# Kernel tuning notes

Measured on AMD Instinct MI355X. Metric: run time of the kernel, lower is better.

Reference implementation:

```python
import jax, jax.numpy as jnp
import numpy as np

D_MODEL, D_STATE, D_CONV, D_INNER, DT_RANK, K = 96, 16, 3, 192, 6, 4
B, H, W = 1, 64, 64


def setup_inputs() -> dict:
    key = jax.random.key(0)
    ks = jax.random.split(key, 10)
    x = jax.random.normal(ks[0], (B, H, W, D_MODEL), jnp.float32)
    in_proj_w = jax.random.normal(ks[1], (2 * D_INNER, D_MODEL), jnp.float32) * 0.02
    conv_w = jax.random.normal(ks[2], (D_INNER, 1, D_CONV, D_CONV), jnp.float32) * 0.1
    conv_b = jnp.zeros((D_INNER,), jnp.float32)
    x_proj_w = jax.random.normal(ks[3], (K, DT_RANK + 2 * D_STATE, D_INNER), jnp.float32) * 0.02
    dt_std = DT_RANK ** -0.5
    dt_w = jax.random.uniform(ks[4], (K, D_INNER, DT_RANK), jnp.float32, -dt_std, dt_std)
    # dt bias init: inv-softplus of dt ~ logUniform(1e-3, 1e-1)
    u = jax.random.uniform(ks[5], (K, D_INNER), jnp.float32)
    dt = jnp.exp(u * (np.log(0.1) - np.log(0.001)) + np.log(0.001)).clip(1e-4)
    dt_b = dt + jnp.log(-jnp.expm1(-dt))
    A_logs = jnp.log(jnp.broadcast_to(jnp.arange(1, D_STATE + 1, dtype=jnp.float32), (K * D_INNER, D_STATE)))
    Ds = jnp.ones((K * D_INNER,), jnp.float32)
    ln_g = jnp.ones((D_INNER,), jnp.float32)
    ln_b = jnp.zeros((D_INNER,), jnp.float32)
    out_proj_w = jax.random.normal(ks[6], (D_MODEL, D_INNER), jnp.float32) * 0.02
    return dict(x=x, in_proj_w=in_proj_w, conv_w=conv_w, conv_b=conv_b, x_proj_w=x_proj_w,
                dt_w=dt_w, dt_b=dt_b, A_logs=A_logs, Ds=Ds, ln_g=ln_g, ln_b=ln_b,
                out_proj_w=out_proj_w)


def _ss2d(x, in_proj_w, conv_w, conv_b, x_proj_w, dt_w, dt_b, A_logs, Ds, ln_g, ln_b, out_proj_w):
    b, h, w, c = x.shape
    L = h * w
    d = conv_w.shape[0]            # d_inner
    n = A_logs.shape[1]            # d_state
    r = dt_w.shape[2]              # dt_rank
    # in_proj + split
    xz = jnp.einsum('bhwc,ec->bhwe', x, in_proj_w)
    xx, z = xz[..., :d], xz[..., d:]
    # depthwise conv (NCHW) + SiLU
    xc = xx.transpose(0, 3, 1, 2)
    pad = (D_CONV - 1) // 2
    xc = jax.lax.conv_general_dilated(xc, conv_w, (1, 1), [(pad, pad), (pad, pad)],
                                      feature_group_count=d) + conv_b[None, :, None, None]
    xc = jax.nn.silu(xc)
    # 4 scan directions: HW, WH, and their reverses
    x_hw = xc.reshape(b, d, L)
    x_wh = xc.transpose(0, 1, 3, 2).reshape(b, d, L)
    xs = jnp.stack([x_hw, x_wh, x_hw[..., ::-1], x_wh[..., ::-1]], axis=1)  # (b,K,d,L)
    x_dbl = jnp.einsum('bkdl,kcd->bkcl', xs, x_proj_w)
    dts, Bs, Cs = x_dbl[:, :, :r], x_dbl[:, :, r:r + n], x_dbl[:, :, r + n:]
    dts = jnp.einsum('bkrl,kdr->bkdl', dts, dt_w)
    delta = jax.nn.softplus(dts + dt_b[None, :, :, None])        # (b,K,d,L)
    A = -jnp.exp(A_logs).reshape(K, d, n)
    # time-major scanned inputs
    dA = jnp.exp(jnp.einsum('bkdl,kdn->lbkdn', delta, A))        # (L,b,K,d,n)
    dBu = jnp.einsum('bkdl,bknl,bkdl->lbkdn', delta, Bs, xs)
    Ct = Cs.transpose(3, 0, 1, 2)                                # (L,b,K,n)
    def step(hst, inp):
        dA_t, dBu_t, C_t = inp
        hst = dA_t * hst + dBu_t
        return hst, jnp.einsum('bkdn,bkn->bkd', hst, C_t)
    h0 = jnp.zeros((b, K, d, n), jnp.float32)
    _, ys = jax.lax.scan(step, h0, (dA, dBu, Ct))                # ys: (L,b,K,d)
    out_y = ys.transpose(1, 2, 3, 0) + xs * Ds.reshape(K, d)[None, :, :, None]
    # recombine directions
    inv = out_y[:, 2:4][..., ::-1]
    y1 = out_y[:, 0]
    y2 = inv[:, 0]
    wh = out_y[:, 1].reshape(b, d, w, h).transpose(0, 1, 3, 2).reshape(b, d, L)
    invwh = inv[:, 1].reshape(b, d, w, h).transpose(0, 1, 3, 2).reshape(b, d, L)
    y = (y1 + y2 + wh + invwh).transpose(0, 2, 1).reshape(b, h, w, d)
    # LayerNorm (eps=1e-5, torch default)
    mu = y.mean(-1, keepdims=True)
    var = ((y - mu) ** 2).mean(-1, keepdims=True)
    y = (y - mu) * jax.lax.rsqrt(var + 1e-5) * ln_g + ln_b
    y = y * jax.nn.silu(z)
    return jnp.einsum('bhwd,cd->bhwc', y, out_proj_w)


def reference(x, in_proj_w, conv_w, conv_b, x_proj_w, dt_w, dt_b, A_logs, Ds, ln_g, ln_b, out_proj_w):
    return _ss2d(x, in_proj_w, conv_w, conv_b, x_proj_w, dt_w, dt_b, A_logs, Ds, ln_g, ln_b, out_proj_w)
```

## Files before the change

### kernel.cpp

```cpp
#include <hip/hip_runtime.h>
#include <hip/hip_bf16.h>

#define LL 4096
#define DM 96
#define DI 192
#define NS 16
#define RK 6
#define RKP 8
#define KD 4
#define CPROJ 38
#define NC (KD*DI*NS)
#define PT 32
#define WS 196
#define OT 16
#define L2E 1.44269504f

__device__ __forceinline__ float b2f(__hip_bfloat16 v){ return __bfloat162float(v); }

__device__ __forceinline__ int detect_bf16(const unsigned short* __restrict__ xh, int tid, int* sflag){
  if (tid < 64){
    unsigned short u = xh[2*tid];
    int e = (u >> 7) & 0xFF;
    int sane = (e >= 107 && e <= 131) ? 1 : 0;
    unsigned long long m = __ballot(sane);
    if (tid == 0) *sflag = (__popcll(m) >= 32) ? 1 : 0;
  }
  return 0;
}

struct P12 { const void* p[12]; };
__global__ void k_convert_all(P12 ptrs, float* __restrict__ dst) {
  const int off[13] = {0,393216,430080,431808,432000,461184,465792,466560,
                       478848,479616,479808,480000,498432};
  __shared__ int sflag;
  detect_bf16((const unsigned short*)ptrs.p[0], threadIdx.x, &sflag);
  __syncthreads();
  int f = sflag;
  int i = blockIdx.x * 256 + threadIdx.x;
  if (i >= 498432) return;
  int j = 0;
  #pragma unroll
  for (int s = 1; s < 12; s++) if (i >= off[s]) j = s;
  int e = i - off[j];
  if (f) dst[i] = b2f(((const __hip_bfloat16*)ptrs.p[j])[e]);
  else   dst[i] = ((const float*)ptrs.p[j])[e];
}

__global__ void k_inproj(const float* __restrict__ x,
                         const float* __restrict__ w,
                         float* __restrict__ xx, float* __restrict__ z) {
  __shared__ float xr[8*DM];
  int l0 = blockIdx.x * 8;
  int tid = threadIdx.x;
  for (int i = tid; i < 8*DM; i += 384) xr[i] = x[l0*DM + i];
  __syncthreads();
  int e = tid;
  float acc[8];
  #pragma unroll
  for (int i=0;i<8;i++) acc[i]=0.f;
  const float* wr = w + e*DM;
  for (int c=0;c<DM;c++){
    float wv = wr[c];
    #pragma unroll
    for (int i=0;i<8;i++) acc[i] = fmaf(wv, xr[i*DM+c], acc[i]);
  }
  if (e < DI) {
    #pragma unroll
    for (int i=0;i<8;i++) xx[(l0+i)*DI + e] = acc[i];
  } else {
    int e2 = e - DI;
    #pragma unroll
    for (int i=0;i<8;i++) z[(l0+i)*DI + e2] = acc[i];
  }
}

__global__ void k_conv(const float* __restrict__ xx,
                       const float* __restrict__ cw,
                       const float* __restrict__ cb,
                       float* __restrict__ xc) {
  int l = blockIdx.x;
  int d = threadIdx.x;
  int h = l >> 6, w = l & 63;
  float acc = cb[d];
  #pragma unroll
  for (int ki=0; ki<3; ki++){
    int hh = h + ki - 1;
    if ((unsigned)hh >= 64u) continue;
    #pragma unroll
    for (int kj=0;kj<3;kj++){
      int wj = w + kj - 1;
      if ((unsigned)wj >= 64u) continue;
      acc = fmaf(cw[d*9 + ki*3 + kj], xx[(hh*64+wj)*DI + d], acc);
    }
  }
  xc[l*DI + d] = acc / (1.f + __expf(-acc));
}

__device__ __forceinline__ int dir_map(int k, int t){
  if (k==0) return t;
  if (k==1) return ((t&63)<<6) | (t>>6);
  if (k==2) return 4095 - t;
  int u = 4095 - t; return ((u&63)<<6) | (u>>6);
}

__global__ void __launch_bounds__(256) k_proj(const float* __restrict__ xc,
                       const float* __restrict__ xpw,
                       float* __restrict__ dts,
                       float* __restrict__ Bb, float* __restrict__ Cb,
                       float* __restrict__ yacc) {
  __shared__ float wl[CPROJ*WS];
  __shared__ float xs[PT*WS];
  int b = blockIdx.x;
  int k = b >> 7;
  int t_base = (b & 127) * PT;
  int tid = threadIdx.x;
  if (k == 0){
    float4* yz = (float4*)(yacc + (size_t)t_base*DI);
    for (int idx = tid; idx < PT*DI/4; idx += 256)
      yz[idx] = make_float4(0.f,0.f,0.f,0.f);
  }
  for (int idx = tid; idx < CPROJ*DI; idx += 256){
    int cc = idx / DI, j = idx - cc*DI;
    wl[cc*WS + j] = xpw[(k*CPROJ + cc)*DI + j];
  }
  for (int idx = tid; idx < PT*DI; idx += 256){
    int tt = idx / DI, j = idx - tt*DI;
    xs[tt*WS + j] = xc[dir_map(k, t_base + tt)*DI + j];
  }
  __syncthreads();
  int tg = tid & 7;
  int ty = tid >> 3;
  int cc0 = ty;
  int has2 = (ty + 32 < CPROJ);
  int cc1 = has2 ? (ty + 32) : ty;
  float a0x=0.f,a0y=0.f,a0z=0.f,a0w=0.f;
  float a1x=0.f,a1y=0.f,a1z=0.f,a1w=0.f;
  const float4* w0p = (const float4*)&wl[cc0*WS];
  const float4* w1p = (const float4*)&wl[cc1*WS];
  const float4* x0p = (const float4*)&xs[(tg     )*WS];
  const float4* x1p = (const float4*)&xs[(tg +  8)*WS];
  const float4* x2p = (const float4*)&xs[(tg + 16)*WS];
  const float4* x3p = (const float4*)&xs[(tg + 24)*WS];
  #pragma unroll 4
  for (int jc = 0; jc < DI/4; jc++){
    float4 w0 = w0p[jc], w1 = w1p[jc];
    float4 x0 = x0p[jc], x1 = x1p[jc], x2 = x2p[jc], x3 = x3p[jc];
    a0x = fmaf(w0.x,x0.x,fmaf(w0.y,x0.y,fmaf(w0.z,x0.z,fmaf(w0.w,x0.w,a0x))));
    a0y = fmaf(w0.x,x1.x,fmaf(w0.y,x1.y,fmaf(w0.z,x1.z,fmaf(w0.w,x1.w,a0y))));
    a0z = fmaf(w0.x,x2.x,fmaf(w0.y,x2.y,fmaf(w0.z,x2.z,fmaf(w0.w,x2.w,a0z))));
    a0w = fmaf(w0.x,x3.x,fmaf(w0.y,x3.y,fmaf(w0.z,x3.z,fmaf(w0.w,x3.w,a0w))));
    a1x = fmaf(w1.x,x0.x,fmaf(w1.y,x0.y,fmaf(w1.z,x0.z,fmaf(w1.w,x0.w,a1x))));
    a1y = fmaf(w1.x,x1.x,fmaf(w1.y,x1.y,fmaf(w1.z,x1.z,fmaf(w1.w,x1.w,a1y))));
    a1z = fmaf(w1.x,x2.x,fmaf(w1.y,x2.y,fmaf(w1.z,x2.z,fmaf(w1.w,x2.w,a1z))));
    a1w = fmaf(w1.x,x3.x,fmaf(w1.y,x3.y,fmaf(w1.z,x3.z,fmaf(w1.w,x3.w,a1w))));
  }
  float accs0[4] = {a0x,a0y,a0z,a0w};
  float accs1[4] = {a1x,a1y,a1z,a1w};
  #pragma unroll
  for (int i=0;i<4;i++){
    int t = t_base + tg + 8*i;
    size_t kt = (size_t)k*LL + t;
    {
      int cc = cc0; float v = accs0[i];
      if (cc < RK)            dts[kt*RKP + cc] = v;
      else if (cc < RK+NS)    Bb [kt*NS + (cc-RK)] = v;
      else                    Cb [kt*NS + (cc-RK-NS)] = v;
    }
    if (has2){
      int cc = ty + 32; float v = accs1[i];
      if (cc < RK+NS)         Bb [kt*NS + (cc-RK)] = v;
      else                    Cb [kt*NS + (cc-RK-NS)] = v;
    }
  }
}

template<int CHB>
__global__ void __launch_bounds__(256) k_scan1(
                      const float* __restrict__ xc,
                      const float* __restrict__ dts,
                      const float* __restrict__ Bbuf,
                      const float* __restrict__ A_logs,
                      const float* __restrict__ dtw,
                      const float* __restrict__ dtb,
                      float* __restrict__ Pb, float* __restrict__ Hb) {
  constexpr int CS = LL >> CHB;
  int b = blockIdx.x;
  int c = b & ((1<<CHB)-1);
  int kg = b >> CHB;
  int k = kg / 3, dg3 = kg - k*3;
  int tid = threadIdx.x;
  int dl = tid >> 2, nq = tid & 3;
  int d = dg3*64 + dl;
  int kd = k*DI + d;
  float4 Al = *(const float4*)&A_logs[kd*NS + nq*4];
  float A0 = -__expf(Al.x)*L2E, A1 = -__expf(Al.y)*L2E;
  float A2 = -__expf(Al.z)*L2E, A3 = -__expf(Al.w)*L2E;
  float bt = dtb[kd];
  float w0 = dtw[kd*RK+0], w1 = dtw[kd*RK+1], w2 = dtw[kd*RK+2];
  float w3 = dtw[kd*RK+3], w4 = dtw[kd*RK+4], w5 = dtw[kd*RK+5];
  const float* dr = dts + ((size_t)k*LL + c*CS)*RKP;
  const float4* bp = (const float4*)(Bbuf + ((size_t)k*LL + c*CS)*NS) + nq;
  float h0=0.f,h1=0.f,h2=0.f,h3=0.f, P0=1.f,P1=1.f,P2=1.f,P3=1.f;
  for (int s=0; s<CS; s++){
    int t = c*CS + s;
    float4 lo = *(const float4*)(dr + s*RKP);
    float4 hi = *(const float4*)(dr + s*RKP + 4);
    float v = bt;
    v = fmaf(w0, lo.x, v); v = fmaf(w1, lo.y, v); v = fmaf(w2, lo.z, v);
    v = fmaf(w3, lo.w, v); v = fmaf(w4, hi.x, v); v = fmaf(w5, hi.y, v);
    float sp = (v > 20.f) ? v : __logf(1.f + __expf(v));
    float sx = sp * xc[dir_map(k,t)*DI + d];
    float4 bv = bp[s*4];
    float a;
    a = exp2f(sp*A0); h0 = fmaf(a, h0, sx*bv.x); P0 *= a;
    a = exp2f(sp*A1); h1 = fmaf(a, h1, sx*bv.y); P1 *= a;
    a = exp2f(sp*A2); h2 = fmaf(a, h2, sx*bv.z); P2 *= a;
    a = exp2f(sp*A3); h3 = fmaf(a, h3, sx*bv.w); P3 *= a;
  }
  int base = c*NC + kd*NS + nq*4;
  *(float4*)&Pb[base] = make_float4(P0,P1,P2,P3);
  *(float4*)&Hb[base] = make_float4(h0,h1,h2,h3);
}

__global__ void __launch_bounds__(256) k_scan2(
                      const float* __restrict__ Pb, float* __restrict__ Hb,
                      int CHn) {
  int idx = blockIdx.x*256 + threadIdx.x;
  float h = 0.f;
  #pragma unroll 4
  for (int c=0;c<CHn;c++){
    float P = Pb[c*NC + idx];
    float Hc = Hb[c*NC + idx];
    Hb[c*NC + idx] = h;
    h = fmaf(P, h, Hc);
  }
}

template<int CHB>
__global__ void __launch_bounds__(256) k_scan3(
                      const float* __restrict__ xc,
                      const float* __restrict__ dts,
                      const float* __restrict__ Bbuf,
                      const float* __restrict__ Cbuf,
                      const float* __restrict__ A_logs,
                      const float* __restrict__ dtw,
                      const float* __restrict__ dtb,
                      const float* __restrict__ H0,
                      float* __restrict__ yacc) {
  constexpr int CS = LL >> CHB;
  int b = blockIdx.x;
  int c = b & ((1<<CHB)-1);
  int kg = b >> CHB;
  int k = kg / 3, dg3 = kg - k*3;
  int tid = threadIdx.x;
  int dl = tid >> 2, nq = tid & 3;
  int d = dg3*64 + dl;
  int kd = k*DI + d;
  float4 Al = *(const float4*)&A_logs[kd*NS + nq*4];
  float A0 = -__expf(Al.x)*L2E, A1 = -__expf(Al.y)*L2E;
  float A2 = -__expf(Al.z)*L2E, A3 = -__expf(Al.w)*L2E;
  float bt = dtb[kd];
  float w0 = dtw[kd*RK+0], w1 = dtw[kd*RK+1], w2 = dtw[kd*RK+2];
  float w3 = dtw[kd*RK+3], w4 = dtw[kd*RK+4], w5 = dtw[kd*RK+5];
  const float* dr = dts + ((size_t)k*LL + c*CS)*RKP;
  const float4* bp = (const float4*)(Bbuf + ((size_t)k*LL + c*CS)*NS) + nq;
  const float4* cp = (const float4*)(Cbuf + ((size_t)k*LL + c*CS)*NS) + nq;
  float4 hv = *(const float4*)&H0[c*NC + kd*NS + nq*4];
  float h0=hv.x, h1=hv.y, h2=hv.z, h3=hv.w;
  for (int s=0; s<CS; s++){
    int t = c*CS + s;
    float4 lo = *(const float4*)(dr + s*RKP);
    float4 hi = *(const float4*)(dr + s*RKP + 4);
    float v = bt;
    v = fmaf(w0, lo.x, v); v = fmaf(w1, lo.y, v); v = fmaf(w2, lo.z, v);
    v = fmaf(w3, lo.w, v); v = fmaf(w4, hi.x, v); v = fmaf(w5, hi.y, v);
    float sp = (v > 20.f) ? v : __logf(1.f + __expf(v));
    int l = dir_map(k,t);
    float sx = sp * xc[l*DI + d];
    float4 bv = bp[s*4];
    float4 cv = cp[s*4];
    float a;
    a = exp2f(sp*A0); h0 = fmaf(a, h0, sx*bv.x);
    a = exp2f(sp*A1); h1 = fmaf(a, h1, sx*bv.y);
    a = exp2f(sp*A2); h2 = fmaf(a, h2, sx*bv.z);
    a = exp2f(sp*A3); h3 = fmaf(a, h3, sx*bv.w);
    float y = h0*cv.x + h1*cv.y + h2*cv.z + h3*cv.w;
    y += __shfl_xor(y, 1, 64);
    y += __shfl_xor(y, 2, 64);
    if (nq == 0) atomicAdd(&yacc[(size_t)l*DI + d], y);
  }
}

__global__ void k_ln(const float* __restrict__ yacc,
                     const float* __restrict__ xc,
                     const float* __restrict__ z,
                     const float* __restrict__ Ds,
                     const float* __restrict__ ln_g,
                     const float* __restrict__ ln_b,
                     float* __restrict__ g) {
  int l = blockIdx.x;
  int d = threadIdx.x;
  float y = yacc[(size_t)l*DI + d];
  float dsum = Ds[0*DI+d] + Ds[1*DI+d] + Ds[2*DI+d] + Ds[3*DI+d];
  y = fmaf(xc[l*DI+d], dsum, y);
  float s1 = y, s2 = y*y;
  #pragma unroll
  for (int off=32; off; off>>=1){
    s1 += __shfl_xor(s1, off, 64);
    s2 += __shfl_xor(s2, off, 64);
  }
  __shared__ float red[6];
  int wave = d >> 6;
  if ((d & 63) == 0){ red[wave] = s1; red[3+wave] = s2; }
  __syncthreads();
  float sum = red[0]+red[1]+red[2];
  float sq  = red[3]+red[4]+red[5];
  float mu = sum * (1.f/192.f);
  float var = sq * (1.f/192.f) - mu*mu;
  float rstd = rsqrtf(var + 1e-5f);
  float yn = (y - mu) * rstd * ln_g[d] + ln_b[d];
  float zv = z[l*DI + d];
  g[(size_t)l*DI + d] = yn * (zv / (1.f + __expf(-zv)));
}

__global__ void __launch_bounds__(192) k_oproj(const float* __restrict__ g,
                      const float* __restrict__ opw,
                      void* __restrict__ out,
                      const unsigned short* __restrict__ xh) {
  __shared__ float gs[OT*WS];
  __shared__ int sflag;
  int tid = threadIdx.x;
  detect_bf16(xh, tid, &sflag);
  int l0 = blockIdx.x * OT;
  const float4* gsrc = (const float4*)(g + (size_t)l0*DI);
  for (int idx = tid; idx < OT*DI/4; idx += 192){
    int row = idx / 48, col = idx - row*48;
    float4 v = gsrc[idx];
    *(float4*)&gs[row*WS + col*4] = v;
  }
  __syncthreads();
  int half = tid / 96;
  int e = tid - half*96;
  int r0 = half*8;
  float acc[8];
  #pragma unroll
  for (int i=0;i<8;i++) acc[i] = 0.f;
  const float4* wrow = (const float4*)(opw + e*DI);
  #pragma unroll 4
  for (int jc = 0; jc < DI/4; jc++){
    float4 w = wrow[jc];
    #pragma unroll
    for (int i=0;i<8;i++){
      float4 gv = *(const float4*)&gs[(r0+i)*WS + jc*4];
      acc[i] = fmaf(w.x,gv.x,fmaf(w.y,gv.y,fmaf(w.z,gv.z,fmaf(w.w,gv.w,acc[i]))));
    }
  }
  int f = sflag;
  #pragma unroll
  for (int i=0;i<8;i++){
    int l = l0 + r0 + i;
    if (f) ((__hip_bfloat16*)out)[l*DM + e] = __float2bfloat16(acc[i]);
    else   ((float*)out)[l*DM + e] = acc[i];
  }
}

extern "C" void kernel_launch(void* const* d_in, const int* in_sizes, int n_in,
                              void* d_out, int out_size, void* d_ws, size_t ws_size,
                              hipStream_t stream) {
  float* ws = (float*)d_ws;
  float* cvt = ws + 16;
  const int off[13] = {0,393216,430080,431808,432000,461184,465792,466560,
                       478848,479616,479808,480000,498432};
  float* c[12];
  for (int i = 0; i < 12; i++) c[i] = cvt + off[i];

  float* big    = cvt + 498432;
  float* xx     = big;
  float* z      = xx + (size_t)LL*DI;
  float* xc     = z  + (size_t)LL*DI;
  float* dts    = xc + (size_t)LL*DI;
  float* Bb     = dts + (size_t)KD*LL*RKP;
  float* Cb     = Bb + (size_t)KD*LL*NS;
  float* Pb     = Cb + (size_t)KD*LL*NS;
  size_t need128 = (size_t)(16 + 498432 + 3*786432 + 131072 + 2*262144 + 2*128*NC) * 4;
  int chBits = (ws_size >= need128) ? 7 : 6;
  int CHn = 1 << chBits;
  float* Hb   = Pb + (size_t)CHn*NC;
  float* yacc = xx;

  P12 ptrs;
  for (int i = 0; i < 12; i++) ptrs.p[i] = d_in[i];
  k_convert_all<<<(498432 + 255)/256, 256, 0, stream>>>(ptrs, cvt);

  k_inproj<<<LL/8, 384, 0, stream>>>(c[0], c[1], xx, z);
  k_conv<<<LL, DI, 0, stream>>>(xx, c[2], c[3], xc);
  k_proj<<<KD*(LL/PT), 256, 0, stream>>>(xc, c[4], dts, Bb, Cb, yacc);
  if (chBits == 7){
    k_scan1<7><<<KD*3*128, 256, 0, stream>>>(xc, dts, Bb, c[7], c[5], c[6], Pb, Hb);
    k_scan2<<<NC/256, 256, 0, stream>>>(Pb, Hb, 128);
    k_scan3<7><<<KD*3*128, 256, 0, stream>>>(xc, dts, Bb, Cb, c[7], c[5], c[6], Hb, yacc);
  } else {
    k_scan1<6><<<KD*3*64, 256, 0, stream>>>(xc, dts, Bb, c[7], c[5], c[6], Pb, Hb);
    k_scan2<<<NC/256, 256, 0, stream>>>(Pb, Hb, 64);
    k_scan3<6><<<KD*3*64, 256, 0, stream>>>(xc, dts, Bb, Cb, c[7], c[5], c[6], Hb, yacc);
  }
  k_ln<<<LL, DI, 0, stream>>>(yacc, xc, z, c[8], c[9], c[10], Hb);
  k_oproj<<<LL/OT, 192, 0, stream>>>(Hb, c[11], d_out, (const unsigned short*)d_in[0]);
}
```

Measured before the change: 213.0 us.

## Precompute softplus delta and delta*x once in a separate kernel for the scans

Adds a k_delta kernel that computes the dt projection, softplus and the sp*x product once per (direction, timestep, channel). It stores the pair as float2 in the workspace. Both scan passes then load this pair instead of recomputing it, which they previously did redundantly in four lanes per channel and again in each pass. The cost is an extra launch plus writing and twice re-reading a roughly 25 MB buffer. The workspace size check now covers this buffer for the 128-chunk path, but the 64-chunk fallback is not checked against it.

```diff
diff --git a/kernel.cpp b/kernel.cpp
--- a/kernel.cpp
+++ b/kernel.cpp
@@ -174,14 +174,42 @@
   }
 }
 
+__global__ void __launch_bounds__(192) k_delta(
+                      const float* __restrict__ dts,
+                      const float* __restrict__ xc,
+                      const float* __restrict__ dtw,
+                      const float* __restrict__ dtb,
+                      float2* __restrict__ spx) {
+  int b = blockIdx.x;
+  int k = b >> 7;
+  int t0 = (b & 127) * 32;
+  int d = threadIdx.x;
+  int kd = k*DI + d;
+  float bt = dtb[kd];
+  float w0 = dtw[kd*RK+0], w1 = dtw[kd*RK+1], w2 = dtw[kd*RK+2];
+  float w3 = dtw[kd*RK+3], w4 = dtw[kd*RK+4], w5 = dtw[kd*RK+5];
+  __shared__ float sd[32*RKP];
+  for (int i = d; i < 32*RKP; i += 192)
+    sd[i] = dts[((size_t)k*LL + t0)*RKP + i];
+  __syncthreads();
+  #pragma unroll 4
+  for (int s = 0; s < 32; s++){
+    int t = t0 + s;
+    float v = bt;
+    v = fmaf(w0, sd[s*RKP+0], v); v = fmaf(w1, sd[s*RKP+1], v);
+    v = fmaf(w2, sd[s*RKP+2], v); v = fmaf(w3, sd[s*RKP+3], v);
+    v = fmaf(w4, sd[s*RKP+4], v); v = fmaf(w5, sd[s*RKP+5], v);
+    float sp = (v > 20.f) ? v : __logf(1.f + __expf(v));
+    float sx = sp * xc[dir_map(k,t)*DI + d];
+    spx[((size_t)k*LL + t)*DI + d] = make_float2(sp, sx);
+  }
+}
+
 template<int CHB>
 __global__ void __launch_bounds__(256) k_scan1(
-                      const float* __restrict__ xc,
-                      const float* __restrict__ dts,
+                      const float2* __restrict__ spx,
                       const float* __restrict__ Bbuf,
                       const float* __restrict__ A_logs,
-                      const float* __restrict__ dtw,
-                      const float* __restrict__ dtb,
                       float* __restrict__ Pb, float* __restrict__ Hb) {
   constexpr int CS = LL >> CHB;
   int b = blockIdx.x;
@@ -195,21 +223,12 @@
   float4 Al = *(const float4*)&A_logs[kd*NS + nq*4];
   float A0 = -__expf(Al.x)*L2E, A1 = -__expf(Al.y)*L2E;
   float A2 = -__expf(Al.z)*L2E, A3 = -__expf(Al.w)*L2E;
-  float bt = dtb[kd];
-  float w0 = dtw[kd*RK+0], w1 = dtw[kd*RK+1], w2 = dtw[kd*RK+2];
-  float w3 = dtw[kd*RK+3], w4 = dtw[kd*RK+4], w5 = dtw[kd*RK+5];
-  const float* dr = dts + ((size_t)k*LL + c*CS)*RKP;
+  const float2* sp_p = spx + ((size_t)k*LL + c*CS)*DI + d;
   const float4* bp = (const float4*)(Bbuf + ((size_t)k*LL + c*CS)*NS) + nq;
   float h0=0.f,h1=0.f,h2=0.f,h3=0.f, P0=1.f,P1=1.f,P2=1.f,P3=1.f;
   for (int s=0; s<CS; s++){
-    int t = c*CS + s;
-    float4 lo = *(const float4*)(dr + s*RKP);
-    float4 hi = *(const float4*)(dr + s*RKP + 4);
-    float v = bt;
-    v = fmaf(w0, lo.x, v); v = fmaf(w1, lo.y, v); v = fmaf(w2, lo.z, v);
-    v = fmaf(w3, lo.w, v); v = fmaf(w4, hi.x, v); v = fmaf(w5, hi.y, v);
-    float sp = (v > 20.f) ? v : __logf(1.f + __expf(v));
-    float sx = sp * xc[dir_map(k,t)*DI + d];
+    float2 sv = sp_p[(size_t)s*DI];
+    float sp = sv.x, sx = sv.y;
     float4 bv = bp[s*4];
     float a;
     a = exp2f(sp*A0); h0 = fmaf(a, h0, sx*bv.x); P0 *= a;
@@ -238,13 +257,10 @@
 
 template<int CHB>
 __global__ void __launch_bounds__(256) k_scan3(
-                      const float* __restrict__ xc,
-                      const float* __restrict__ dts,
+                      const float2* __restrict__ spx,
                       const float* __restrict__ Bbuf,
                       const float* __restrict__ Cbuf,
                       const float* __restrict__ A_logs,
-                      const float* __restrict__ dtw,
-                      const float* __restrict__ dtb,
                       const float* __restrict__ H0,
                       float* __restrict__ yacc) {
   constexpr int CS = LL >> CHB;
@@ -259,24 +275,15 @@
   float4 Al = *(const float4*)&A_logs[kd*NS + nq*4];
   float A0 = -__expf(Al.x)*L2E, A1 = -__expf(Al.y)*L2E;
   float A2 = -__expf(Al.z)*L2E, A3 = -__expf(Al.w)*L2E;
-  float bt = dtb[kd];
-  float w0 = dtw[kd*RK+0], w1 = dtw[kd*RK+1], w2 = dtw[kd*RK+2];
-  float w3 = dtw[kd*RK+3], w4 = dtw[kd*RK+4], w5 = dtw[kd*RK+5];
-  const float* dr = dts + ((size_t)k*LL + c*CS)*RKP;
+  const float2* sp_p = spx + ((size_t)k*LL + c*CS)*DI + d;
   const float4* bp = (const float4*)(Bbuf + ((size_t)k*LL + c*CS)*NS) + nq;
   const float4* cp = (const float4*)(Cbuf + ((size_t)k*LL + c*CS)*NS) + nq;
   float4 hv = *(const float4*)&H0[c*NC + kd*NS + nq*4];
   float h0=hv.x, h1=hv.y, h2=hv.z, h3=hv.w;
   for (int s=0; s<CS; s++){
     int t = c*CS + s;
-    float4 lo = *(const float4*)(dr + s*RKP);
-    float4 hi = *(const float4*)(dr + s*RKP + 4);
-    float v = bt;
-    v = fmaf(w0, lo.x, v); v = fmaf(w1, lo.y, v); v = fmaf(w2, lo.z, v);
-    v = fmaf(w3, lo.w, v); v = fmaf(w4, hi.x, v); v = fmaf(w5, hi.y, v);
-    float sp = (v > 20.f) ? v : __logf(1.f + __expf(v));
-    int l = dir_map(k,t);
-    float sx = sp * xc[l*DI + d];
+    float2 sv = sp_p[(size_t)s*DI];
+    float sp = sv.x, sx = sv.y;
     float4 bv = bp[s*4];
     float4 cv = cp[s*4];
     float a;
@@ -287,7 +294,7 @@
     float y = h0*cv.x + h1*cv.y + h2*cv.z + h3*cv.w;
     y += __shfl_xor(y, 1, 64);
     y += __shfl_xor(y, 2, 64);
-    if (nq == 0) atomicAdd(&yacc[(size_t)l*DI + d], y);
+    if (nq == 0) atomicAdd(&yacc[(size_t)dir_map(k,t)*DI + d], y);
   }
 }
 
@@ -382,10 +389,12 @@
   float* Bb     = dts + (size_t)KD*LL*RKP;
   float* Cb     = Bb + (size_t)KD*LL*NS;
   float* Pb     = Cb + (size_t)KD*LL*NS;
-  size_t need128 = (size_t)(16 + 498432 + 3*786432 + 131072 + 2*262144 + 2*128*NC) * 4;
+  size_t need128 = (size_t)(16 + 498432 + 3*786432 + 131072 + 2*262144
+                            + 2*128*NC + 2*(size_t)KD*LL*DI) * 4;
   int chBits = (ws_size >= need128) ? 7 : 6;
   int CHn = 1 << chBits;
   float* Hb   = Pb + (size_t)CHn*NC;
+  float2* spx = (float2*)(Hb + (size_t)CHn*NC);
   float* yacc = xx;
 
   P12 ptrs;
@@ -395,14 +404,15 @@
   k_inproj<<<LL/8, 384, 0, stream>>>(c[0], c[1], xx, z);
   k_conv<<<LL, DI, 0, stream>>>(xx, c[2], c[3], xc);
   k_proj<<<KD*(LL/PT), 256, 0, stream>>>(xc, c[4], dts, Bb, Cb, yacc);
+  k_delta<<<KD*128, 192, 0, stream>>>(dts, xc, c[5], c[6], spx);
   if (chBits == 7){
-    k_scan1<7><<<KD*3*128, 256, 0, stream>>>(xc, dts, Bb, c[7], c[5], c[6], Pb, Hb);
+    k_scan1<7><<<KD*3*128, 256, 0, stream>>>(spx, Bb, c[7], Pb, Hb);
     k_scan2<<<NC/256, 256, 0, stream>>>(Pb, Hb, 128);
-    k_scan3<7><<<KD*3*128, 256, 0, stream>>>(xc, dts, Bb, Cb, c[7], c[5], c[6], Hb, yacc);
+    k_scan3<7><<<KD*3*128, 256, 0, stream>>>(spx, Bb, Cb, c[7], Hb, yacc);
   } else {
-    k_scan1<6><<<KD*3*64, 256, 0, stream>>>(xc, dts, Bb, c[7], c[5], c[6], Pb, Hb);
+    k_scan1<6><<<KD*3*64, 256, 0, stream>>>(spx, Bb, c[7], Pb, Hb);
     k_scan2<<<NC/256, 256, 0, stream>>>(Pb, Hb, 64);
-    k_scan3<6><<<KD*3*64, 256, 0, stream>>>(xc, dts, Bb, Cb, c[7], c[5], c[6], Hb, yacc);
+    k_scan3<6><<<KD*3*64, 256, 0, stream>>>(spx, Bb, Cb, c[7], Hb, yacc);
   }
   k_ln<<<LL, DI, 0, stream>>>(yacc, xc, z, c[8], c[9], c[10], Hb);
   k_oproj<<<LL/OT, 192, 0, stream>>>(Hb, c[11], d_out, (const unsigned short*)d_in[0]);
```

After: 214.7 us. About the same (+0.8%).

## Replace two-pass chunked scan with single pass plus carry-in correction kernel

Applied to the files above, without the earlier changes.

The chunked selective scan now runs the full recurrence once from zero state per chunk. That pass emits partial outputs, the chunk decay product (computed from the cumulative delta sum) and the per-step cumulative delta. A new correction kernel adds each chunk's carry-in contribution C·exp(A·cumDelta)·h_in to the output. This removes the second full recurrence pass over the sequence. In exchange it writes and reads a large per-step cumulative-delta buffer and does extra exp2 work and atomics in the correction kernel.

```diff
diff --git a/kernel.cpp b/kernel.cpp
--- a/kernel.cpp
+++ b/kernel.cpp
@@ -179,73 +179,12 @@
                       const float* __restrict__ xc,
                       const float* __restrict__ dts,
                       const float* __restrict__ Bbuf,
-                      const float* __restrict__ A_logs,
-                      const float* __restrict__ dtw,
-                      const float* __restrict__ dtb,
-                      float* __restrict__ Pb, float* __restrict__ Hb) {
-  constexpr int CS = LL >> CHB;
-  int b = blockIdx.x;
-  int c = b & ((1<<CHB)-1);
-  int kg = b >> CHB;
-  int k = kg / 3, dg3 = kg - k*3;
-  int tid = threadIdx.x;
-  int dl = tid >> 2, nq = tid & 3;
-  int d = dg3*64 + dl;
-  int kd = k*DI + d;
-  float4 Al = *(const float4*)&A_logs[kd*NS + nq*4];
-  float A0 = -__expf(Al.x)*L2E, A1 = -__expf(Al.y)*L2E;
-  float A2 = -__expf(Al.z)*L2E, A3 = -__expf(Al.w)*L2E;
-  float bt = dtb[kd];
-  float w0 = dtw[kd*RK+0], w1 = dtw[kd*RK+1], w2 = dtw[kd*RK+2];
-  float w3 = dtw[kd*RK+3], w4 = dtw[kd*RK+4], w5 = dtw[kd*RK+5];
-  const float* dr = dts + ((size_t)k*LL + c*CS)*RKP;
-  const float4* bp = (const float4*)(Bbuf + ((size_t)k*LL + c*CS)*NS) + nq;
-  float h0=0.f,h1=0.f,h2=0.f,h3=0.f, P0=1.f,P1=1.f,P2=1.f,P3=1.f;
-  for (int s=0; s<CS; s++){
-    int t = c*CS + s;
-    float4 lo = *(const float4*)(dr + s*RKP);
-    float4 hi = *(const float4*)(dr + s*RKP + 4);
-    float v = bt;
-    v = fmaf(w0, lo.x, v); v = fmaf(w1, lo.y, v); v = fmaf(w2, lo.z, v);
-    v = fmaf(w3, lo.w, v); v = fmaf(w4, hi.x, v); v = fmaf(w5, hi.y, v);
-    float sp = (v > 20.f) ? v : __logf(1.f + __expf(v));
-    float sx = sp * xc[dir_map(k,t)*DI + d];
-    float4 bv = bp[s*4];
-    float a;
-    a = exp2f(sp*A0); h0 = fmaf(a, h0, sx*bv.x); P0 *= a;
-    a = exp2f(sp*A1); h1 = fmaf(a, h1, sx*bv.y); P1 *= a;
-    a = exp2f(sp*A2); h2 = fmaf(a, h2, sx*bv.z); P2 *= a;
-    a = exp2f(sp*A3); h3 = fmaf(a, h3, sx*bv.w); P3 *= a;
-  }
-  int base = c*NC + kd*NS + nq*4;
-  *(float4*)&Pb[base] = make_float4(P0,P1,P2,P3);
-  *(float4*)&Hb[base] = make_float4(h0,h1,h2,h3);
-}
-
-__global__ void __launch_bounds__(256) k_scan2(
-                      const float* __restrict__ Pb, float* __restrict__ Hb,
-                      int CHn) {
-  int idx = blockIdx.x*256 + threadIdx.x;
-  float h = 0.f;
-  #pragma unroll 4
-  for (int c=0;c<CHn;c++){
-    float P = Pb[c*NC + idx];
-    float Hc = Hb[c*NC + idx];
-    Hb[c*NC + idx] = h;
-    h = fmaf(P, h, Hc);
-  }
-}
-
-template<int CHB>
-__global__ void __launch_bounds__(256) k_scan3(
-                      const float* __restrict__ xc,
-                      const float* __restrict__ dts,
-                      const float* __restrict__ Bbuf,
                       const float* __restrict__ Cbuf,
                       const float* __restrict__ A_logs,
                       const float* __restrict__ dtw,
                       const float* __restrict__ dtb,
-                      const float* __restrict__ H0,
+                      float* __restrict__ Pb, float* __restrict__ Hb,
+                      float* __restrict__ SDb,
                       float* __restrict__ yacc) {
   constexpr int CS = LL >> CHB;
   int b = blockIdx.x;
@@ -265,8 +204,7 @@
   const float* dr = dts + ((size_t)k*LL + c*CS)*RKP;
   const float4* bp = (const float4*)(Bbuf + ((size_t)k*LL + c*CS)*NS) + nq;
   const float4* cp = (const float4*)(Cbuf + ((size_t)k*LL + c*CS)*NS) + nq;
-  float4 hv = *(const float4*)&H0[c*NC + kd*NS + nq*4];
-  float h0=hv.x, h1=hv.y, h2=hv.z, h3=hv.w;
+  float h0=0.f,h1=0.f,h2=0.f,h3=0.f, cumD=0.f;
   for (int s=0; s<CS; s++){
     int t = c*CS + s;
     float4 lo = *(const float4*)(dr + s*RKP);
@@ -275,6 +213,7 @@
     v = fmaf(w0, lo.x, v); v = fmaf(w1, lo.y, v); v = fmaf(w2, lo.z, v);
     v = fmaf(w3, lo.w, v); v = fmaf(w4, hi.x, v); v = fmaf(w5, hi.y, v);
     float sp = (v > 20.f) ? v : __logf(1.f + __expf(v));
+    cumD += sp;
     int l = dir_map(k,t);
     float sx = sp * xc[l*DI + d];
     float4 bv = bp[s*4];
@@ -287,7 +226,69 @@
     float y = h0*cv.x + h1*cv.y + h2*cv.z + h3*cv.w;
     y += __shfl_xor(y, 1, 64);
     y += __shfl_xor(y, 2, 64);
-    if (nq == 0) atomicAdd(&yacc[(size_t)l*DI + d], y);
+    if (nq == 0){
+      atomicAdd(&yacc[(size_t)l*DI + d], y);
+      SDb[(size_t)(k*LL + t)*DI + d] = cumD;
+    }
+  }
+  int base = c*NC + kd*NS + nq*4;
+  *(float4*)&Pb[base] = make_float4(exp2f(A0*cumD), exp2f(A1*cumD),
+                                    exp2f(A2*cumD), exp2f(A3*cumD));
+  *(float4*)&Hb[base] = make_float4(h0,h1,h2,h3);
+}
+
+__global__ void __launch_bounds__(256) k_scan2(
+                      const float* __restrict__ Pb, float* __restrict__ Hb,
+                      int CHn) {
+  int idx = blockIdx.x*256 + threadIdx.x;
+  float h = 0.f;
+  #pragma unroll 4
+  for (int c=0;c<CHn;c++){
+    float P = Pb[c*NC + idx];
+    float Hc = Hb[c*NC + idx];
+    Hb[c*NC + idx] = h;
+    h = fmaf(P, h, Hc);
+  }
+}
+
+template<int CHB>
+__global__ void __launch_bounds__(192) k_corr(
+                      const float* __restrict__ Cbuf,
+                      const float* __restrict__ A_logs,
+                      const float* __restrict__ Hb,
+                      const float* __restrict__ SDb,
+                      float* __restrict__ yacc) {
+  int b = blockIdx.x;
+  int k = b >> 7;
+  int t0 = (b & 127) * 32;
+  int c = t0 >> (12 - CHB);
+  if (c == 0) return;
+  int d = threadIdx.x;
+  int kd = k*DI + d;
+  __shared__ float cs[32*NS];
+  for (int i = d; i < 32*NS; i += 192)
+    cs[i] = Cbuf[((size_t)k*LL + t0)*NS + i];
+  float A2[16], he[16];
+  {
+    const float4* ap = (const float4*)&A_logs[kd*NS];
+    const float4* hp = (const float4*)&Hb[c*NC + kd*NS];
+    #pragma unroll
+    for (int i=0;i<4;i++){
+      float4 av = ap[i];
+      A2[4*i+0] = -__expf(av.x)*L2E; A2[4*i+1] = -__expf(av.y)*L2E;
+      A2[4*i+2] = -__expf(av.z)*L2E; A2[4*i+3] = -__expf(av.w)*L2E;
+      *(float4*)&he[4*i] = hp[i];
+    }
+  }
+  __syncthreads();
+  for (int s=0; s<32; s++){
+    int t = t0 + s;
+    float SD = SDb[(size_t)(k*LL + t)*DI + d];
+    float corr = 0.f;
+    #pragma unroll
+    for (int n=0;n<16;n++)
+      corr = fmaf(cs[s*NS+n]*exp2f(A2[n]*SD), he[n], corr);
+    atomicAdd(&yacc[(size_t)dir_map(k,t)*DI + d], corr);
   }
 }
 
@@ -382,10 +383,12 @@
   float* Bb     = dts + (size_t)KD*LL*RKP;
   float* Cb     = Bb + (size_t)KD*LL*NS;
   float* Pb     = Cb + (size_t)KD*LL*NS;
-  size_t need128 = (size_t)(16 + 498432 + 3*786432 + 131072 + 2*262144 + 2*128*NC) * 4;
+  size_t need128 = (size_t)(16 + 498432 + 3*786432 + 131072 + 2*262144
+                            + 2*128*NC + (size_t)KD*LL*DI) * 4;
   int chBits = (ws_size >= need128) ? 7 : 6;
   int CHn = 1 << chBits;
   float* Hb   = Pb + (size_t)CHn*NC;
+  float* SDb  = Hb + (size_t)CHn*NC;
   float* yacc = xx;
 
   P12 ptrs;
@@ -396,13 +399,13 @@
   k_conv<<<LL, DI, 0, stream>>>(xx, c[2], c[3], xc);
   k_proj<<<KD*(LL/PT), 256, 0, stream>>>(xc, c[4], dts, Bb, Cb, yacc);
   if (chBits == 7){
-    k_scan1<7><<<KD*3*128, 256, 0, stream>>>(xc, dts, Bb, c[7], c[5], c[6], Pb, Hb);
+    k_scan1<7><<<KD*3*128, 256, 0, stream>>>(xc, dts, Bb, Cb, c[7], c[5], c[6], Pb, Hb, SDb, yacc);
     k_scan2<<<NC/256, 256, 0, stream>>>(Pb, Hb, 128);
-    k_scan3<7><<<KD*3*128, 256, 0, stream>>>(xc, dts, Bb, Cb, c[7], c[5], c[6], Hb, yacc);
+    k_corr<7><<<KD*128, 192, 0, stream>>>(Cb, c[7], Hb, SDb, yacc);
   } else {
-    k_scan1<6><<<KD*3*64, 256, 0, stream>>>(xc, dts, Bb, c[7], c[5], c[6], Pb, Hb);
+    k_scan1<6><<<KD*3*64, 256, 0, stream>>>(xc, dts, Bb, Cb, c[7], c[5], c[6], Pb, Hb, SDb, yacc);
     k_scan2<<<NC/256, 256, 0, stream>>>(Pb, Hb, 64);
-    k_scan3<6><<<KD*3*64, 256, 0, stream>>>(xc, dts, Bb, Cb, c[7], c[5], c[6], Hb, yacc);
+    k_corr<6><<<KD*128, 192, 0, stream>>>(Cb, c[7], Hb, SDb, yacc);
   }
   k_ln<<<LL, DI, 0, stream>>>(yacc, xc, z, c[8], c[9], c[10], Hb);
   k_oproj<<<LL/OT, 192, 0, stream>>>(Hb, c[11], d_out, (const unsigned short*)d_in[0]);
```

New measurement: 216.8 us. About the same (+1.8%).
